# Kernel tuning notes

Hardware: AMD Instinct MI355X
Metric: run time of the kernel (lower is better)

## Reference

```python
import jax, jax.numpy as jnp
import numpy as np
from jax import lax

H, W = 96, 96          # PNet output map size
STRIDE, CELL = 2, 12   # PNet stride / receptive cell
SCALE = 12.0 / 20.0    # first pyramid scale = net_size / min_face_size
THR_SCORE = 0.6        # threshold[0]
THR_NMS = 0.5          # per-scale NMS threshold in detect_pnet


def setup_inputs() -> dict:
    key = jax.random.key(0)
    k1, k2 = jax.random.split(key)
    cls_prob = jax.random.uniform(k1, (H, W), dtype=jnp.float32)
    bbox_pred = jax.random.normal(k2, (H, W, 4), dtype=jnp.float32) * 0.1
    return {"cls_prob": cls_prob, "bbox_pred": bbox_pred}


def _nms_keep(boxes, scores, mask, thr):
    """Greedy NMS over N boxes with validity mask; returns bool keep mask [N]."""
    N = scores.shape[0]
    # invalid boxes sort last
    order = jnp.argsort(-jnp.where(mask, scores, -jnp.inf))
    b = boxes[order]
    m = mask[order]
    x1, y1, x2, y2 = b[:, 0], b[:, 1], b[:, 2], b[:, 3]
    areas = (x2 - x1 + 1.0) * (y2 - y1 + 1.0)
    # pairwise IoU [N, N]
    xx1 = jnp.maximum(x1[:, None], x1[None, :])
    yy1 = jnp.maximum(y1[:, None], y1[None, :])
    xx2 = jnp.minimum(x2[:, None], x2[None, :])
    yy2 = jnp.minimum(y2[:, None], y2[None, :])
    inter = jnp.maximum(xx2 - xx1 + 1.0, 0.0) * jnp.maximum(yy2 - yy1 + 1.0, 0.0)
    iou = inter / (areas[:, None] + areas[None, :] - inter)
    idx = jnp.arange(N)

    def step(keep, xs):
        i, iou_row, m_i = xs
        suppressed = jnp.any(keep & (iou_row > thr) & (idx < i))
        k_i = m_i & jnp.logical_not(suppressed)
        keep = keep.at[i].set(k_i)
        return keep, None

    keep_sorted, _ = lax.scan(step, jnp.zeros((N,), bool), (idx, iou, m))
    return jnp.zeros((N,), bool).at[order].set(keep_sorted)


def reference(cls_prob, bbox_pred):
    # generate_bbox: decode grid anchors back to original-image coords
    rows, cols = jnp.meshgrid(jnp.arange(H, dtype=jnp.float32),
                              jnp.arange(W, dtype=jnp.float32), indexing="ij")
    x1 = jnp.round(STRIDE * cols / SCALE).reshape(-1)
    y1 = jnp.round(STRIDE * rows / SCALE).reshape(-1)
    x2 = jnp.round((STRIDE * cols + CELL) / SCALE).reshape(-1)
    y2 = jnp.round((STRIDE * rows + CELL) / SCALE).reshape(-1)
    score = cls_prob.reshape(-1)
    reg = bbox_pred.reshape(-1, 4)
    mask = score > THR_SCORE

    boxes5 = jnp.stack([x1, y1, x2, y2, score], axis=-1)  # [N,5]
    keep = _nms_keep(boxes5[:, :4], score, mask, THR_NMS)

    bbw = x2 - x1 + 1.0
    bbh = y2 - y1 + 1.0
    boxes_c = jnp.stack([x1 + reg[:, 0] * bbw,
                         y1 + reg[:, 1] * bbh,
                         x2 + reg[:, 2] * bbw,
                         y2 + reg[:, 3] * bbh,
                         score], axis=-1)  # [N,5]
    return boxes_c * keep[:, None].astype(boxes_c.dtype)
```

## Files before the change

### kernel.cpp

```cpp
#include <hip/hip_runtime.h>


namespace {

constexpr int Hh = 96, Ww = 96, Nn = Hh * Ww;
constexpr int NW = Nn / 64;
constexpr float THR_SCORE = 0.6f;
constexpr int NT = 512;


__device__ __forceinline__ unsigned long long shift_b(const unsigned long long w[9], int b) {
  switch (b) {
    case 0:  return (w[4] << 1)  | (w[3] >> 63);
    case 1:  return (w[4] >> 1)  | (w[5] << 63);
    case 2:  return (w[4] << 2)  | (w[3] >> 62);
    case 3:  return (w[4] >> 2)  | (w[5] << 62);
    case 4:  return (w[3] << 32) | (w[2] >> 32);
    case 5:  return (w[5] >> 32) | (w[6] << 32);
    case 6:  return w[1];
    case 7:  return w[7];
    case 8:  return (w[3] << 33) | (w[2] >> 31);
    case 9:  return (w[3] << 31) | (w[2] >> 33);
    case 10: return (w[5] >> 31) | (w[6] << 33);
    default: return (w[5] >> 33) | (w[6] << 31);
  }
}

__global__ __launch_bounds__(NT) void mtcnn_kernel(
    const float* __restrict__ cls,
    const float* __restrict__ bbox,
    float* __restrict__ out)
{
  __shared__ float s_sc[Nn];
  __shared__ unsigned long long s_D[12][NW];
  __shared__ unsigned long long s_Up[NW + 8];
  __shared__ unsigned long long s_Kp[NW + 8];
  __shared__ float s_lo[Ww], s_hi[Ww];
  __shared__ int s_ch[3];

  unsigned long long* const U = s_Up + 4;
  unsigned long long* const K = s_Kp + 4;

  const int tid = threadIdx.x;
  const int lane = tid & 63;
  const int OFF[12] = {-1, 1, -2, 2, -Ww, Ww, -2*Ww, 2*Ww, -Ww-1, -Ww+1, Ww-1, Ww+1};

  if (tid < Ww) {
    float c = (float)tid;
    s_lo[tid] = rintf((2.0f * c) / 0.6f);
    s_hi[tid] = rintf((2.0f * c + 12.0f) / 0.6f);
  }
  for (int q = tid; q < Nn / 4; q += NT)
    reinterpret_cast<float4*>(s_sc)[q] = reinterpret_cast<const float4*>(cls)[q];
  if (tid < 4) {
    s_Up[tid] = 0ull; s_Kp[tid] = 0ull;
    s_Up[4 + NW + tid] = 0ull; s_Kp[4 + NW + tid] = 0ull;
  }
  if (tid < 3) s_ch[tid] = 0;
  __syncthreads();

  for (int n = tid; n < Nn; n += NT) {
    float si = s_sc[n];
    unsigned int m = 0;
    bool valid = si > THR_SCORE;
    if (valid) {
      int r = n / Ww, c = n - r * Ww;
      int rm = r % 3, cm = c % 3;
      unsigned int geom = (1u << 0) | (1u << 1) | (1u << 4) | (1u << 5);
      if (cm == 1) geom |= 1u << 2;
      if (cm == 2) geom |= 1u << 3;
      if (rm == 1) geom |= 1u << 6;
      if (rm == 2) geom |= 1u << 7;
      if (!(rm == 2 && cm == 2)) geom |= 1u << 8;
      if (!(rm == 2 && cm == 1)) geom |= 1u << 9;
      if (!(rm == 1 && cm == 2)) geom |= 1u << 10;
      if (!(rm == 1 && cm == 1)) geom |= 1u << 11;
      unsigned int inb = 0;
      bool cge1 = c >= 1, cle = c <= Ww - 2, rge1 = r >= 1, rle = r <= Hh - 2;
      if (cge1) inb |= 1u << 0;
      if (cle)  inb |= 1u << 1;
      if (c >= 2)      inb |= 1u << 2;
      if (c <= Ww - 3) inb |= 1u << 3;
      if (rge1) inb |= 1u << 4;
      if (rle)  inb |= 1u << 5;
      if (r >= 2)      inb |= 1u << 6;
      if (r <= Hh - 3) inb |= 1u << 7;
      if (rge1 && cge1) inb |= 1u << 8;
      if (rge1 && cle)  inb |= 1u << 9;
      if (rle && cge1)  inb |= 1u << 10;
      if (rle && cle)   inb |= 1u << 11;
      unsigned int cand = geom & inb;
      #pragma unroll
      for (int b = 0; b < 12; ++b) {
        int j = n + OFF[b];
        j = min(max(j, 0), Nn - 1);
        float sj = s_sc[j];
        bool ge = (b == 0) | (b == 2) | (b == 4) | (b == 6) | (b == 8) | (b == 9);
        bool dom = ge ? (sj >= si) : (sj > si);
        if (((cand >> b) & 1u) && (sj > THR_SCORE) && dom) m |= 1u << b;
      }
    }
    int w = n >> 6;
    #pragma unroll
    for (int b = 0; b < 12; ++b) {
      unsigned long long bb = __ballot((m >> b) & 1u);
      if (lane == 0) s_D[b][w] = bb;
    }
    unsigned long long vb = __ballot(valid);
    if (lane == 0) { U[w] = vb; K[w] = 0ull; }
  }
  __syncthreads();

  for (int it = 0; it < 9999; ++it) {
    const int f = it % 3;
    if (tid == 0) s_ch[(it + 1) % 3] = 0;
    if (tid < NW) {
      const int t = tid;
      unsigned long long u = U[t];
      if (u) {
        unsigned long long wu[9], wk[9];
        #pragma unroll
        for (int j = 0; j < 9; ++j) { wu[j] = U[t - 4 + j]; wk[j] = K[t - 4 + j]; }
        unsigned long long anyK = 0ull, anyU = 0ull;
        #pragma unroll
        for (int b = 0; b < 12; ++b) {
          unsigned long long d = s_D[b][t];
          anyK |= shift_b(wk, b) & d;
          anyU |= shift_b(wu, b) & d;
        }
        unsigned long long u2 = u & anyU & ~anyK;
        if (u2 != u) {
          K[t] = wk[4] | (u & ~anyU & ~anyK);
          U[t] = u2;
          s_ch[f] = 1;
        }
      }
    }
    __syncthreads();
    if (s_ch[f] == 0) break;
  }

  for (int n = tid; n < Nn; n += NT) {
    int r = n / Ww, c = n - r * Ww;
    float x1 = s_lo[c], x2 = s_hi[c], y1 = s_lo[r], y2 = s_hi[r];
    float k = (float)((K[n >> 6] >> (n & 63)) & 1ull);
    float bbw = x2 - x1 + 1.0f, bbh = y2 - y1 + 1.0f;
    float4 reg = reinterpret_cast<const float4*>(bbox)[n];
    out[n * 5 + 0] = (x1 + reg.x * bbw) * k;
    out[n * 5 + 1] = (y1 + reg.y * bbh) * k;
    out[n * 5 + 2] = (x2 + reg.z * bbw) * k;
    out[n * 5 + 3] = (y2 + reg.w * bbh) * k;
    out[n * 5 + 4] = s_sc[n] * k;
  }
}

}

extern "C" void kernel_launch(void* const* d_in, const int* in_sizes, int n_in,
                              void* d_out, int out_size, void* d_ws, size_t ws_size,
                              hipStream_t stream) {
  const float* cls  = (const float*)d_in[0];
  const float* bbox = (const float*)d_in[1];
  float* out = (float*)d_out;
  hipLaunchKernelGGL(mtcnn_kernel, dim3(1), dim3(NT), 0, stream, cls, bbox, out);
}
```

Baseline: 84.68 us.

## Keep NMS state in registers, double threads, vectorize output stores

Raises the block size from 512 to 1024 threads. Each word-owner thread keeps its own 12 dominance masks and its own undecided/kept words in registers across the iterative suppression loop, so only neighbour words are read from LDS. The output phase now writes float4 chunks of the 5-float rows and recomputes box coordinates inline instead of reading a shared table. In exchange, each output chunk needs redundant work for two cells plus select logic, and the larger block may raise register pressure; the loop cap also drops to 3000 iterations.

New measurement: 92.79 us. 1.1x slower.

```diff
diff --git a/kernel.cpp b/kernel.cpp
--- a/kernel.cpp
+++ b/kernel.cpp
@@ -6,8 +6,7 @@
 constexpr int Hh = 96, Ww = 96, Nn = Hh * Ww;
 constexpr int NW = Nn / 64;
 constexpr float THR_SCORE = 0.6f;
-constexpr int NT = 512;
-
+constexpr int NT = 1024;
 
 __device__ __forceinline__ unsigned long long shift_b(const unsigned long long w[9], int b) {
   switch (b) {
@@ -26,6 +25,12 @@
   }
 }
 
+struct Cell5 { float a, b, c, d, e; };
+
+__device__ __forceinline__ float pick5(const Cell5& s, int j) {
+  return j == 0 ? s.a : j == 1 ? s.b : j == 2 ? s.c : j == 3 ? s.d : s.e;
+}
+
 __global__ __launch_bounds__(NT) void mtcnn_kernel(
     const float* __restrict__ cls,
     const float* __restrict__ bbox,
@@ -35,7 +40,6 @@
   __shared__ unsigned long long s_D[12][NW];
   __shared__ unsigned long long s_Up[NW + 8];
   __shared__ unsigned long long s_Kp[NW + 8];
-  __shared__ float s_lo[Ww], s_hi[Ww];
   __shared__ int s_ch[3];
 
   unsigned long long* const U = s_Up + 4;
@@ -45,11 +49,6 @@
   const int lane = tid & 63;
   const int OFF[12] = {-1, 1, -2, 2, -Ww, Ww, -2*Ww, 2*Ww, -Ww-1, -Ww+1, Ww-1, Ww+1};
 
-  if (tid < Ww) {
-    float c = (float)tid;
-    s_lo[tid] = rintf((2.0f * c) / 0.6f);
-    s_hi[tid] = rintf((2.0f * c + 12.0f) / 0.6f);
-  }
   for (int q = tid; q < Nn / 4; q += NT)
     reinterpret_cast<float4*>(s_sc)[q] = reinterpret_cast<const float4*>(cls)[q];
   if (tid < 4) {
@@ -111,46 +110,77 @@
   }
   __syncthreads();
 
-  for (int it = 0; it < 9999; ++it) {
+  const int t = tid;
+  unsigned long long regD[12];
+  unsigned long long u_self = 0ull, k_self = 0ull;
+  if (t < NW) {
+    #pragma unroll
+    for (int b = 0; b < 12; ++b) regD[b] = s_D[b][t];
+    u_self = U[t];
+  }
+  for (int it = 0; it < 3000; ++it) {
     const int f = it % 3;
     if (tid == 0) s_ch[(it + 1) % 3] = 0;
-    if (tid < NW) {
-      const int t = tid;
-      unsigned long long u = U[t];
-      if (u) {
-        unsigned long long wu[9], wk[9];
-        #pragma unroll
-        for (int j = 0; j < 9; ++j) { wu[j] = U[t - 4 + j]; wk[j] = K[t - 4 + j]; }
-        unsigned long long anyK = 0ull, anyU = 0ull;
-        #pragma unroll
-        for (int b = 0; b < 12; ++b) {
-          unsigned long long d = s_D[b][t];
-          anyK |= shift_b(wk, b) & d;
-          anyU |= shift_b(wu, b) & d;
-        }
-        unsigned long long u2 = u & anyU & ~anyK;
-        if (u2 != u) {
-          K[t] = wk[4] | (u & ~anyU & ~anyK);
-          U[t] = u2;
-          s_ch[f] = 1;
-        }
+    if (t < NW && u_self) {
+      unsigned long long wu[9], wk[9];
+      #pragma unroll
+      for (int j = 0; j < 9; ++j) {
+        if (j == 4) continue;
+        wu[j] = U[t - 4 + j]; wk[j] = K[t - 4 + j];
+      }
+      wu[4] = u_self; wk[4] = k_self;
+      unsigned long long anyK = 0ull, anyU = 0ull;
+      #pragma unroll
+      for (int b = 0; b < 12; ++b) {
+        anyK |= shift_b(wk, b) & regD[b];
+        anyU |= shift_b(wu, b) & regD[b];
+      }
+      unsigned long long u2 = u_self & anyU & ~anyK;
+      if (u2 != u_self) {
+        k_self |= u_self & ~anyU & ~anyK;
+        u_self = u2;
+        U[t] = u_self; K[t] = k_self;
+        s_ch[f] = 1;
       }
     }
     __syncthreads();
     if (s_ch[f] == 0) break;
   }
 
-  for (int n = tid; n < Nn; n += NT) {
-    int r = n / Ww, c = n - r * Ww;
-    float x1 = s_lo[c], x2 = s_hi[c], y1 = s_lo[r], y2 = s_hi[r];
-    float k = (float)((K[n >> 6] >> (n & 63)) & 1ull);
-    float bbw = x2 - x1 + 1.0f, bbh = y2 - y1 + 1.0f;
-    float4 reg = reinterpret_cast<const float4*>(bbox)[n];
-    out[n * 5 + 0] = (x1 + reg.x * bbw) * k;
-    out[n * 5 + 1] = (y1 + reg.y * bbh) * k;
-    out[n * 5 + 2] = (x2 + reg.z * bbw) * k;
-    out[n * 5 + 3] = (y2 + reg.w * bbh) * k;
-    out[n * 5 + 4] = s_sc[n] * k;
+  const float4* bbox4 = reinterpret_cast<const float4*>(bbox);
+  float4* out4 = reinterpret_cast<float4*>(out);
+  for (int q = tid; q < (Nn * 5) / 4; q += NT) {
+    int e = q * 4;
+    int n0 = e / 5;
+    int j0 = e - n0 * 5;
+    int n1 = (j0 <= 1) ? n0 : (n0 + 1);
+    Cell5 v0, v1;
+    #pragma unroll
+    for (int s = 0; s < 2; ++s) {
+      int n = s ? n1 : n0;
+      int r = n / Ww, c = n - r * Ww;
+      float fc = (float)c, fr = (float)r;
+      float x1 = rintf((2.0f * fc) / 0.6f);
+      float x2 = rintf((2.0f * fc + 12.0f) / 0.6f);
+      float y1 = rintf((2.0f * fr) / 0.6f);
+      float y2 = rintf((2.0f * fr + 12.0f) / 0.6f);
+      float k = (float)((K[n >> 6] >> (n & 63)) & 1ull);
+      float4 reg = bbox4[n];
+      float bw = x2 - x1 + 1.0f, bh = y2 - y1 + 1.0f;
+      Cell5 v;
+      v.a = (x1 + reg.x * bw) * k;
+      v.b = (y1 + reg.y * bh) * k;
+      v.c = (x2 + reg.z * bw) * k;
+      v.d = (y2 + reg.w * bh) * k;
+      v.e = s_sc[n] * k;
+      if (s) v1 = v; else v0 = v;
+    }
+    float4 o;
+    o.x = (j0 + 0 < 5) ? pick5(v0, j0 + 0) : pick5(v1, j0 - 5);
+    o.y = (j0 + 1 < 5) ? pick5(v0, j0 + 1) : pick5(v1, j0 - 4);
+    o.z = (j0 + 2 < 5) ? pick5(v0, j0 + 2) : pick5(v1, j0 - 3);
+    o.w = (j0 + 3 < 5) ? pick5(v0, j0 + 3) : pick5(v1, j0 - 2);
+    out4[q] = o;
   }
 }
 
```
